# Performance work log

Measured on AMD Instinct MI355X. Metric: run time of the kernel, lower is better.

Reference implementation:

```python
import jax, jax.numpy as jnp
import numpy as np

N, D = 16384, 512
MARGIN = 2.0
EPS = 1e-6  # torch TripletMarginLoss default eps added inside pairwise distance


def setup_inputs() -> dict:
    key = jax.random.key(0)
    k1, k2 = jax.random.split(key)
    inputs = jax.random.normal(k1, (N, D), dtype=jnp.float32)
    positive = jax.random.normal(k2, (N, D), dtype=jnp.float32)
    return {"inputs": inputs, "positive": positive}


def reference(inputs, positive):
    # pairwise squared euclidean distances: ||xi||^2 + ||xj||^2 - 2 xi.xj
    sq = jnp.sum(inputs * inputs, axis=1)                      # [n]
    dist2 = sq[:, None] + sq[None, :] - 2.0 * (inputs @ inputs.T)  # [n,n]
    dist = jnp.sqrt(jnp.clip(dist2, 1e-12))                    # [n,n]
    # original does full argsort per row but only uses index 2 (3rd smallest);
    # top_k on negated distances selects the 3 smallest efficiently.
    _, idx3 = jax.lax.top_k(-dist, 3)                          # [n,3]
    negative = inputs[idx3[:, 2]]                              # [n,d]
    # TripletMarginLoss(margin, p=2): mean(relu(||a-p+eps|| - ||a-n+eps|| + m))
    d_ap = jnp.linalg.norm(inputs - positive + EPS, axis=1)
    d_an = jnp.linalg.norm(inputs - negative + EPS, axis=1)
    loss = jnp.mean(jnp.maximum(d_ap - d_an + MARGIN, 0.0))
    return loss
```

## Files before the change

### kernel.cpp

```cpp
#include <hip/hip_runtime.h>
#include <hip/hip_bf16.h>
#include <hip/hip_fp8.h>
#include <stdint.h>

#define NN 16384
#define DD 512
#define MARGINV 2.0f
#define EPSV 1e-6f

#define BJ 32
#define JGROUPS 8
#define JRANGE (NN / JGROUPS)
#define NTILES (JRANGE / BJ)
#define ROWQ 512
#define TILEB (BJ * ROWQ)
#define SQOFF (2 * TILEB)

#define KEYMASK  0xFFFFC000
#define KEYINITF __builtin_bit_cast(float, 0x7F000000)
#define BIASV 640.0f

typedef __attribute__((ext_vector_type(4))) float f32x4;
typedef __attribute__((ext_vector_type(4))) int   i32x4;
typedef __attribute__((ext_vector_type(8))) int   i32x8;

#define UNIT_SCALE 0x7F

__device__ inline void kins2f(float u, float& m0, float& m1) {
  m1 = __builtin_amdgcn_fmed3f(m0, m1, u);
  m0 = fminf(m0, u);
}

extern "C" __global__ __launch_bounds__(256)
void prep_kernel(const float* __restrict__ x, unsigned char* __restrict__ xq,
                 float* __restrict__ sqb) {
  int row  = blockIdx.x * 4 + (threadIdx.x >> 6);
  int lane = threadIdx.x & 63;
  const float* xr = x + (size_t)row * DD + lane * 8;
  f32x4 a = *(const f32x4*)xr;
  f32x4 b = *(const f32x4*)(xr + 4);
  float s = a[0]*a[0]+a[1]*a[1]+a[2]*a[2]+a[3]*a[3]
          + b[0]*b[0]+b[1]*b[1]+b[2]*b[2]+b[3]*b[3];
  #pragma unroll
  for (int off = 1; off < 64; off <<= 1) s += __shfl_xor(s, off, 64);
  unsigned int w0 = (unsigned int)__builtin_amdgcn_cvt_pk_fp8_f32(a[0], a[1], 0, false);
  w0 = (unsigned int)__builtin_amdgcn_cvt_pk_fp8_f32(a[2], a[3], (int)w0, true);
  unsigned int w1 = (unsigned int)__builtin_amdgcn_cvt_pk_fp8_f32(b[0], b[1], 0, false);
  w1 = (unsigned int)__builtin_amdgcn_cvt_pk_fp8_f32(b[2], b[3], (int)w1, true);
  unsigned long long pk8 = ((unsigned long long)w1 << 32) | (unsigned long long)w0;
  *(unsigned long long*)(xq + (size_t)row * ROWQ + lane * 8) = pk8;
  if (lane == 0) sqb[row] = s + BIASV;
}

extern "C" __global__ __launch_bounds__(256, 2)
void knn_kernel(const unsigned char* __restrict__ xq, const float* __restrict__ sqb,
                int* __restrict__ pk) {
  __shared__ __align__(16) char lds[2 * TILEB + 8192];
  const int tid  = threadIdx.x;
  const int wave = tid >> 6;
  const int lane = tid & 63;
  const int quad = lane >> 4;
  const int r16  = lane & 15;
  const int bi   = blockIdx.x >> 3;
  const int bj   = blockIdx.x & 7;
  const int ibase = bi * 256 + wave * 64;
  const int jbase = bj * JRANGE;

  #pragma unroll
  for (int p = 0; p < 2; ++p) {
    const float* gs = sqb + jbase + p * 1024 + wave * 256 + lane * 4;
    char* ld = lds + SQOFF + p * 4096 + wave * 1024;
    __builtin_amdgcn_global_load_lds((const __attribute__((address_space(1))) void*)gs,
                                     (__attribute__((address_space(3))) void*)ld,
                                     16, 0, 0);
  }

  i32x8 afr[4][4];
  #pragma unroll
  for (int s = 0; s < 4; ++s) {
    const unsigned char* ar = xq + (size_t)(ibase + s * 16 + r16) * ROWQ + quad * 32;
    #pragma unroll
    for (int c = 0; c < 4; ++c)
      afr[s][c] = *(const i32x8*)(ar + c * 128);
  }

  float m0[16], m1[16];
  #pragma unroll
  for (int q = 0; q < 16; ++q) { m0[q] = m1[q] = KEYINITF; }

  auto stage = [&](int jt, int buf) {
    const int jrow0 = jbase + jt * BJ;
    #pragma unroll
    for (int p = 0; p < 4; ++p) {
      const int rr = wave * 8 + p * 2;
      const int lr = rr + (lane >> 5);
      const int u  = (lane & 31) ^ (lr & 7);
      const unsigned char* gsrc = xq + (size_t)(jrow0 + lr) * ROWQ + u * 16;
      char* ldst = lds + buf * TILEB + rr * ROWQ;
      __builtin_amdgcn_global_load_lds((const __attribute__((address_space(1))) void*)gsrc,
                                       (__attribute__((address_space(3))) void*)ldst,
                                       16, 0, 0);
    }
  };

  const int sw = r16 & 7;
  stage(0, 0);
  for (int jt = 0; jt < NTILES; ++jt) {
    __syncthreads();
    if (jt + 1 < NTILES) stage(jt + 1, (jt + 1) & 1);
    #pragma unroll
    for (int jh = 0; jh < 2; ++jh) {
      const char* brow = lds + (jt & 1) * TILEB + (jh * 16 + r16) * ROWQ;
      const float sqj = *(const float*)(lds + SQOFF + ((jt * BJ + jh * 16 + r16) << 2));
      f32x4 acc[4] = {{0.f,0.f,0.f,0.f},{0.f,0.f,0.f,0.f},
                      {0.f,0.f,0.f,0.f},{0.f,0.f,0.f,0.f}};
      #pragma unroll
      for (int c = 0; c < 4; ++c) {
        const int g0 = c * 8 + quad * 2;
        i32x4 lo = *(const i32x4*)(brow + ((g0       ^ sw) * 16));
        i32x4 hi = *(const i32x4*)(brow + (((g0 + 1) ^ sw) * 16));
        i32x8 bf = i32x8{lo[0],lo[1],lo[2],lo[3],hi[0],hi[1],hi[2],hi[3]};
        #pragma unroll
        for (int s = 0; s < 4; ++s)
          acc[s] = __builtin_amdgcn_mfma_scale_f32_16x16x128_f8f6f4(
                     afr[s][c], bf, acc[s], 0, 0, 0, UNIT_SCALE, 0, UNIT_SCALE);
      }
      const int j = jbase + jt * BJ + jh * 16 + r16;
      const int jrel = j - ibase - quad * 4;
      #pragma unroll
      for (int s = 0; s < 4; ++s)
      #pragma unroll
      for (int r = 0; r < 4; ++r) {
        float v = fmaf(-2.0f, acc[s][r], sqj);
        int   b = (__builtin_bit_cast(int, v) & KEYMASK) | j;
        float u = __builtin_bit_cast(float, b);
        u = (jrel == (s * 16 + r)) ? KEYINITF : u;
        kins2f(u, m0[s*4+r], m1[s*4+r]);
      }
    }
  }

  #pragma unroll
  for (int m = 1; m <= 8; m <<= 1) {
    #pragma unroll
    for (int q = 0; q < 16; ++q) {
      float o0 = __shfl_xor(m0[q], m, 64);
      float o1 = __shfl_xor(m1[q], m, 64);
      kins2f(o0, m0[q], m1[q]);
      kins2f(o1, m0[q], m1[q]);
    }
  }

  #pragma unroll
  for (int q = 0; q < 16; ++q) {
    if (r16 == q) {
      int s  = q >> 2, r = q & 3;
      int gi = ibase + s * 16 + quad * 4 + r;
      int ob = (gi * JGROUPS + bj) * 2;
      pk[ob + 0] = __builtin_bit_cast(int, m0[q]);
      pk[ob + 1] = __builtin_bit_cast(int, m1[q]);
    }
  }
}

extern "C" __global__ __launch_bounds__(256)
void finalize_kernel(const float* __restrict__ x, const float* __restrict__ pos,
                     const int* __restrict__ pk, float* __restrict__ partial) {
  __shared__ float wsum[4];
  int wave = threadIdx.x >> 6;
  int lane = threadIdx.x & 63;
  float acc = 0.f;
  #pragma unroll
  for (int rep = 0; rep < 2; ++rep) {
    int i = rep * 8192 + blockIdx.x * 4 + wave;
    float m0 = (lane < 16) ? __builtin_bit_cast(float, pk[i * 16 + lane]) : KEYINITF;
    float m1 = KEYINITF;
    #pragma unroll
    for (int m = 1; m <= 8; m <<= 1) {
      float o0 = __shfl_xor(m0, m, 64);
      float o1 = __shfl_xor(m1, m, 64);
      float t0 = fminf(m0, o0);
      m1 = fminf(fmaxf(m0, o0), fminf(m1, o1));
      m0 = t0;
    }
    int neg = __shfl(__builtin_bit_cast(int, m1), 0, 64) & 0x3FFF;
    const float* xr = x   + (size_t)i * DD + lane * 8;
    const float* pr = pos + (size_t)i * DD + lane * 8;
    const float* nr = x   + (size_t)neg * DD + lane * 8;
    f32x4 xa = *(const f32x4*)xr, xb4 = *(const f32x4*)(xr + 4);
    f32x4 pa = *(const f32x4*)pr, pb  = *(const f32x4*)(pr + 4);
    f32x4 na = *(const f32x4*)nr, nb  = *(const f32x4*)(nr + 4);
    float sap = 0.f, san = 0.f;
    #pragma unroll
    for (int k = 0; k < 4; ++k) {
      float d0 = xa[k]  - pa[k] + EPSV; sap = fmaf(d0, d0, sap);
      float d1 = xa[k]  - na[k] + EPSV; san = fmaf(d1, d1, san);
      float d2 = xb4[k] - pb[k] + EPSV; sap = fmaf(d2, d2, sap);
      float d3 = xb4[k] - nb[k] + EPSV; san = fmaf(d3, d3, san);
    }
    #pragma unroll
    for (int off = 1; off < 64; off <<= 1) {
      sap += __shfl_xor(sap, off, 64);
      san += __shfl_xor(san, off, 64);
    }
    if (lane == 0) {
      float l = sqrtf(sap) - sqrtf(san) + MARGINV;
      acc += (l > 0.f ? l : 0.f);
    }
  }
  if (lane == 0) wsum[wave] = acc;
  __syncthreads();
  if (threadIdx.x == 0) partial[blockIdx.x] = wsum[0] + wsum[1] + wsum[2] + wsum[3];
}

extern "C" __global__ __launch_bounds__(256)
void reduce_kernel(const float* __restrict__ partial, float* __restrict__ out) {
  __shared__ float wsum[4];
  int tid = threadIdx.x;
  float s = 0.f;
  #pragma unroll
  for (int k = 0; k < 8; ++k) s += partial[tid + k * 256];
  #pragma unroll
  for (int off = 1; off < 64; off <<= 1) s += __shfl_xor(s, off, 64);
  if ((tid & 63) == 0) wsum[tid >> 6] = s;
  __syncthreads();
  if (tid == 0) out[0] = (wsum[0] + wsum[1] + wsum[2] + wsum[3]) * (1.0f / NN);
}

extern "C" void kernel_launch(void* const* d_in, const int* in_sizes, int n_in,
                              void* d_out, int out_size, void* d_ws, size_t ws_size,
                              hipStream_t stream) {
  const float* x   = (const float*)d_in[0];
  const float* pos = (const float*)d_in[1];
  char* ws = (char*)d_ws;
  unsigned char* xq   = (unsigned char*)ws;
  float* sqb  = (float*)(ws + (size_t)NN * ROWQ);
  int*   pk   = (int*)  (ws + (size_t)NN * ROWQ + (size_t)NN * 4);
  float* part = (float*)(ws + (size_t)NN * ROWQ + (size_t)NN * 4
                            + (size_t)NN * JGROUPS * 2 * 4);

  prep_kernel<<<NN / 4, 256, 0, stream>>>(x, xq, sqb);
  knn_kernel<<<(NN / 256) * JGROUPS, 256, 0, stream>>>(xq, sqb, pk);
  finalize_kernel<<<2048, 256, 0, stream>>>(x, pos, pk, part);
  reduce_kernel<<<1, 256, 0, stream>>>(part, (float*)d_out);
}
```

Measured before the change: 228.0 us.

## Switch kNN distance matmul from FP8 to FP6 E2M3 scaled MFMA

Quantizes inputs to FP6 E2M3 in the prep kernel, packing 32 values into 24 bytes per lane group. The MFMA then runs with FP6 format selectors. This targets the higher FP6 MFMA throughput and makes fewer LDS and register bytes per operand. The row stride and LDS tile layout stay the same, so memory traffic is mostly unchanged. E2M3 has a small range (max 7.5) and coarse precision, which can change which neighbour is chosen as the third nearest.

```diff
diff --git a/kernel.cpp b/kernel.cpp
--- a/kernel.cpp
+++ b/kernel.cpp
@@ -22,13 +22,25 @@
 
 typedef __attribute__((ext_vector_type(4))) float f32x4;
 typedef __attribute__((ext_vector_type(4))) int   i32x4;
+typedef __attribute__((ext_vector_type(2))) int   i32x2;
 typedef __attribute__((ext_vector_type(8))) int   i32x8;
 
 #define UNIT_SCALE 0x7F
+#define FMT_FP6 2
 
 __device__ inline void kins2f(float u, float& m0, float& m1) {
   m1 = __builtin_amdgcn_fmed3f(m0, m1, u);
   m0 = fminf(m0, u);
+}
+
+__device__ inline unsigned int enc_e2m3(float v) {
+  float a = fabsf(v);
+  unsigned int s = (__builtin_bit_cast(unsigned int, v) >> 31) << 5;
+  float c;
+  if (a < 1.9375f)     c = __builtin_rintf(a * 8.0f);
+  else if (a < 3.875f) c = 16.0f + __builtin_rintf((a - 2.0f) * 4.0f);
+  else                 c = 24.0f + __builtin_rintf(fminf((a - 4.0f) * 2.0f, 7.0f));
+  return s | (unsigned int)c;
 }
 
 extern "C" __global__ __launch_bounds__(256)
@@ -37,18 +49,23 @@
   int row  = blockIdx.x * 4 + (threadIdx.x >> 6);
   int lane = threadIdx.x & 63;
   const float* xr = x + (size_t)row * DD + lane * 8;
-  f32x4 a = *(const f32x4*)xr;
-  f32x4 b = *(const f32x4*)(xr + 4);
-  float s = a[0]*a[0]+a[1]*a[1]+a[2]*a[2]+a[3]*a[3]
-          + b[0]*b[0]+b[1]*b[1]+b[2]*b[2]+b[3]*b[3];
+  f32x4 va = *(const f32x4*)xr;
+  f32x4 vb = *(const f32x4*)(xr + 4);
+  float s = va[0]*va[0]+va[1]*va[1]+va[2]*va[2]+va[3]*va[3]
+          + vb[0]*vb[0]+vb[1]*vb[1]+vb[2]*vb[2]+vb[3]*vb[3];
   #pragma unroll
   for (int off = 1; off < 64; off <<= 1) s += __shfl_xor(s, off, 64);
-  unsigned int w0 = (unsigned int)__builtin_amdgcn_cvt_pk_fp8_f32(a[0], a[1], 0, false);
-  w0 = (unsigned int)__builtin_amdgcn_cvt_pk_fp8_f32(a[2], a[3], (int)w0, true);
-  unsigned int w1 = (unsigned int)__builtin_amdgcn_cvt_pk_fp8_f32(b[0], b[1], 0, false);
-  w1 = (unsigned int)__builtin_amdgcn_cvt_pk_fp8_f32(b[2], b[3], (int)w1, true);
-  unsigned long long pk8 = ((unsigned long long)w1 << 32) | (unsigned long long)w0;
-  *(unsigned long long*)(xq + (size_t)row * ROWQ + lane * 8) = pk8;
+  unsigned long long pk6 = 0;
+  #pragma unroll
+  for (int t = 0; t < 4; ++t) {
+    pk6 |= ((unsigned long long)enc_e2m3(va[t])) << (6 * t);
+    pk6 |= ((unsigned long long)enc_e2m3(vb[t])) << (6 * (t + 4));
+  }
+  unsigned char* dst = xq + (size_t)row * ROWQ
+                     + (lane >> 4) * 128 + ((lane >> 2) & 3) * 32 + (lane & 3) * 6;
+  *(unsigned short*)(dst + 0) = (unsigned short)(pk6);
+  *(unsigned short*)(dst + 2) = (unsigned short)(pk6 >> 16);
+  *(unsigned short*)(dst + 4) = (unsigned short)(pk6 >> 32);
   if (lane == 0) sqb[row] = s + BIASV;
 }
 
@@ -75,13 +92,16 @@
                                      16, 0, 0);
   }
 
-  i32x8 afr[4][4];
+  i32x4 afr4[4][4];
+  i32x2 afr2[4][4];
   #pragma unroll
   for (int s = 0; s < 4; ++s) {
     const unsigned char* ar = xq + (size_t)(ibase + s * 16 + r16) * ROWQ + quad * 32;
     #pragma unroll
-    for (int c = 0; c < 4; ++c)
-      afr[s][c] = *(const i32x8*)(ar + c * 128);
+    for (int c = 0; c < 4; ++c) {
+      afr4[s][c] = *(const i32x4*)(ar + c * 128);
+      afr2[s][c] = *(const i32x2*)(ar + c * 128 + 16);
+    }
   }
 
   float m0[16], m1[16];
@@ -118,12 +138,15 @@
       for (int c = 0; c < 4; ++c) {
         const int g0 = c * 8 + quad * 2;
         i32x4 lo = *(const i32x4*)(brow + ((g0       ^ sw) * 16));
-        i32x4 hi = *(const i32x4*)(brow + (((g0 + 1) ^ sw) * 16));
-        i32x8 bf = i32x8{lo[0],lo[1],lo[2],lo[3],hi[0],hi[1],hi[2],hi[3]};
+        i32x2 hi = *(const i32x2*)(brow + (((g0 + 1) ^ sw) * 16));
+        i32x8 bf = i32x8{lo[0],lo[1],lo[2],lo[3],hi[0],hi[1],0,0};
         #pragma unroll
-        for (int s = 0; s < 4; ++s)
+        for (int s = 0; s < 4; ++s) {
+          i32x8 af = i32x8{afr4[s][c][0],afr4[s][c][1],afr4[s][c][2],afr4[s][c][3],
+                           afr2[s][c][0],afr2[s][c][1],0,0};
           acc[s] = __builtin_amdgcn_mfma_scale_f32_16x16x128_f8f6f4(
-                     afr[s][c], bf, acc[s], 0, 0, 0, UNIT_SCALE, 0, UNIT_SCALE);
+                     af, bf, acc[s], FMT_FP6, FMT_FP6, 0, UNIT_SCALE, 0, UNIT_SCALE);
+        }
       }
       const int j = jbase + jt * BJ + jh * 16 + r16;
       const int jrel = j - ibase - quad * 4;
```

Result: faster. 214.0 us (-6.2%).
